# Optimization experiments

Hardware: AMD Instinct MI355X
Metric: run time of the kernel (lower is better)

## Reference

```python
import jax, jax.numpy as jnp
import numpy as np

B, N, D, H = 4, 4096, 512, 8
K = D // H  # per-head dim = 64


def setup_inputs() -> dict:
    key = jax.random.key(0)
    k1, k2, k3, k4 = jax.random.split(key, 4)
    x = jax.random.normal(k1, (B, N, D), dtype=jnp.float32)
    # Conv1d(D, K, 1, bias=False) -> weight matrix [K, D], kaiming fan_out
    Wa = jax.random.normal(k2, (K, D), dtype=jnp.float32) * np.float32(np.sqrt(2.0 / K))
    # Conv1d(K, 1, 1) -> weight vector [K], bias scalar (init 0.01)
    Wb = jax.random.normal(k3, (K,), dtype=jnp.float32) * np.float32(np.sqrt(2.0))
    Wc = jax.random.normal(k4, (K,), dtype=jnp.float32) * np.float32(np.sqrt(2.0))
    wb_bias = jnp.full((), 0.01, dtype=jnp.float32)
    wc_bias = jnp.full((), 0.01, dtype=jnp.float32)
    bias = jnp.full((K,), 0.01, dtype=jnp.float32)
    return {"batchinput": x, "Wa": Wa, "Wb": Wb, "wb_bias": wb_bias,
            "Wc": Wc, "wc_bias": wc_bias, "bias": bias}


def reference(batchinput, Wa, Wb, wb_bias, Wc, wc_bias, bias):
    # single step (n_steps=1); all n_head heads share weights, so mean over
    # identical heads equals one head (dropout=0.0 -> identity).
    h = jnp.einsum('bnd,kd->bnk', batchinput, Wa)            # [B,N,K] projected feats
    t1 = jnp.einsum('bnk,k->bn', h, Wb) + wb_bias            # [B,N]
    t2 = jnp.einsum('bnk,k->bn', h, Wc) + wc_bias            # [B,N]
    scores = t1[:, :, None] + t2[:, None, :]                 # [B,N,N] additive score
    coefs = jax.nn.softmax(jax.nn.leaky_relu(scores, negative_slope=0.2), axis=-1)
    out = jnp.einsum('bnm,bmk->bnk', coefs, h) + bias        # [B,N,K]
    return out
```

## Files before the change

### kernel.cpp

```cpp
#include <hip/hip_runtime.h>
#include <hip/hip_bf16.h>

constexpr int cB = 4;
constexpr int cN = 4096;
constexpr int cD = 512;
constexpr int cK = 64;
constexpr int cNB = cB * cN;
constexpr int cNP = cN + 1;
constexpr int cCS = 16;
constexpr int cNC = cN / cCS;
constexpr int cNC1 = cNC + 1;

typedef unsigned short u16;
typedef unsigned int u32;
typedef unsigned long long u64;
typedef __bf16 bf16x8 __attribute__((ext_vector_type(8)));
typedef float f32x4 __attribute__((ext_vector_type(4)));

constexpr size_t OFF_H    = 0;
constexpr size_t OFF_T1   = OFF_H    + (size_t)cNB * cK;
constexpr size_t OFF_T2   = OFF_T1   + cNB;
constexpr size_t OFF_T2S  = OFF_T2   + cNB;
constexpr size_t OFF_IDX  = OFF_T2S  + cNB;
constexpr size_t OFF_EPL  = OFF_IDX  + cNB;
constexpr size_t OFF_GNL  = OFF_EPL  + (size_t)cB * cNP * cK;
constexpr size_t OFF_EPS  = OFF_GNL  + (size_t)cB * cNP * cK;
constexpr size_t OFF_GNS  = OFF_EPS  + (size_t)cB * cNP;
constexpr size_t OFF_CHE  = OFF_GNS  + (size_t)cB * cNP;
constexpr size_t OFF_CHG  = OFF_CHE  + (size_t)cB * cNC * cK;
constexpr size_t OFF_CHES = OFF_CHG  + (size_t)cB * cNC * cK;
constexpr size_t OFF_CHGS = OFF_CHES + (size_t)cB * cNC;
constexpr size_t OFF_OFE  = OFF_CHGS + (size_t)cB * cNC;
constexpr size_t OFF_OFG  = OFF_OFE  + (size_t)cB * cNC1 * cK;
constexpr size_t OFF_OFES = OFF_OFG  + (size_t)cB * cNC1 * cK;
constexpr size_t OFF_OFGS = OFF_OFES + (size_t)cB * cNC1;
constexpr size_t OFF_XB16 = OFF_OFGS + (size_t)cB * cNC1;
constexpr size_t OFF_WB16 = OFF_XB16 + (size_t)cNB * cD / 2;

__device__ __forceinline__ u16 f2bf(float f) {
    unsigned u = __float_as_uint(f);
    u += 0x7fffu + ((u >> 16) & 1u);
    return (u16)(u >> 16);
}
__device__ __forceinline__ u32 pk2(float a, float b) {
    return (u32)f2bf(a) | ((u32)f2bf(b) << 16);
}
__device__ __forceinline__ u32 f2sort(float f) {
    u32 b = __float_as_uint(f);
    u32 mask = (u32)((int)b >> 31);
    return b ^ (mask | 0x80000000u);
}

__global__ __launch_bounds__(256) void k_prep(
    const float* __restrict__ x, const float* __restrict__ Wa,
    const float* __restrict__ Wb, const float* __restrict__ wbb,
    const float* __restrict__ Wc, const float* __restrict__ wcb,
    u16* __restrict__ xb16, u16* __restrict__ wab16,
    float* __restrict__ t1, float* __restrict__ t2)
{
    __shared__ float wabL[cD], wacL[cD];
    int t = threadIdx.x;
    if (blockIdx.x >= 512) {
        int i4 = (((int)blockIdx.x - 512) * 256 + t) * 4;
        float4 v = *(const float4*)(Wa + i4);
        uint2 p = {pk2(v.x, v.y), pk2(v.z, v.w)};
        *(uint2*)(wab16 + i4) = p;
        return;
    }
    float s1a = 0.f, s2a = 0.f, s1b = 0.f, s2b = 0.f;
#pragma unroll 8
    for (int k = 0; k < cK; ++k) {
        float wbk = Wb[k], wck = Wc[k];
        float wa1 = Wa[k * cD + t];
        float wa2 = Wa[k * cD + t + 256];
        s1a += wa1 * wbk; s2a += wa1 * wck;
        s1b += wa2 * wbk; s2b += wa2 * wck;
    }
    wabL[t] = s1a; wacL[t] = s2a; wabL[t + 256] = s1b; wacL[t + 256] = s2b;
    __syncthreads();

    int w = t >> 6, lane = t & 63;
    int d1 = lane * 4, d2 = 256 + lane * 4;
    float4 wbA = *(const float4*)&wabL[d1], wbB = *(const float4*)&wabL[d2];
    float4 wcA = *(const float4*)&wacL[d1], wcB = *(const float4*)&wacL[d2];
    float wbbv = wbb[0], wcbv = wcb[0];
#pragma unroll 2
    for (int rr = 0; rr < 8; ++rr) {
        int row = blockIdx.x * 32 + w * 8 + rr;
        const float* xp = x + (size_t)row * cD;
        float4 a  = *(const float4*)(xp + d1);
        float4 bq = *(const float4*)(xp + d2);
        uint2 pa = {pk2(a.x, a.y), pk2(a.z, a.w)};
        uint2 pb = {pk2(bq.x, bq.y), pk2(bq.z, bq.w)};
        *(uint2*)(xb16 + (size_t)row * cD + d1) = pa;
        *(uint2*)(xb16 + (size_t)row * cD + d2) = pb;
        float p1 = a.x*wbA.x + a.y*wbA.y + a.z*wbA.z + a.w*wbA.w
                 + bq.x*wbB.x + bq.y*wbB.y + bq.z*wbB.z + bq.w*wbB.w;
        float p2 = a.x*wcA.x + a.y*wcA.y + a.z*wcA.z + a.w*wcA.w
                 + bq.x*wcB.x + bq.y*wcB.y + bq.z*wcB.z + bq.w*wcB.w;
#pragma unroll
        for (int off = 32; off > 0; off >>= 1) {
            p1 += __shfl_down(p1, off, 64);
            p2 += __shfl_down(p2, off, 64);
        }
        if (lane == 0) { t1[row] = p1 + wbbv; t2[row] = p2 + wcbv; }
    }
}

__global__ __launch_bounds__(256) void k_projrank(
    const u16* __restrict__ xb16, const u16* __restrict__ wab16,
    const float* __restrict__ t2,
    float* __restrict__ h, float* __restrict__ t2s, int* __restrict__ idxs)
{
    __shared__ u64 shbuf[4096 + 128];
    int t = threadIdx.x;
    if (blockIdx.x < 256) {
        u16* xs = (u16*)shbuf;
        u16* was = xs + 64 * 32;
        int rowbase = blockIdx.x * 64;
        int w = t >> 6, lane = t & 63, m = lane & 15, quad = lane >> 4;
        int grow = w * 16 + (lane >> 2);
        int gcol = (lane & 3) * 8;
        const u16* xg = xb16 + (size_t)(rowbase + grow) * cD + gcol;
        const u16* wg = wab16 + (size_t)grow * cD + gcol;
        int lidx = grow * 32 + gcol;

        f32x4 acc[4] = {{0.f,0.f,0.f,0.f},{0.f,0.f,0.f,0.f},
                        {0.f,0.f,0.f,0.f},{0.f,0.f,0.f,0.f}};
        uint4 xv = *(const uint4*)(xg);
        uint4 wv = *(const uint4*)(wg);
        for (int s = 0; s < 16; ++s) {
            __syncthreads();
            *(uint4*)&xs[lidx] = xv;
            *(uint4*)&was[lidx] = wv;
            if (s < 15) {
                xv = *(const uint4*)(xg + (s + 1) * 32);
                wv = *(const uint4*)(wg + (s + 1) * 32);
            }
            __syncthreads();
            bf16x8 av = *(const bf16x8*)&xs[(w * 16 + m) * 32 + quad * 8];
#pragma unroll
            for (int g = 0; g < 4; ++g) {
                bf16x8 bv = *(const bf16x8*)&was[(g * 16 + m) * 32 + quad * 8];
                acc[g] = __builtin_amdgcn_mfma_f32_16x16x32_bf16(av, bv, acc[g], 0, 0, 0);
            }
        }
#pragma unroll
        for (int g = 0; g < 4; ++g) {
#pragma unroll
            for (int r4 = 0; r4 < 4; ++r4) {
                int row = w * 16 + quad * 4 + r4;
                h[(size_t)(rowbase + row) * cK + g * 16 + m] = acc[g][r4];
            }
        }
    } else {
        u64* keys = shbuf;
        int* part = (int*)(shbuf + 4096);
        int rb = blockIdx.x - 256;
        int b = rb >> 6;
        int rowgrp = rb & 63;
        for (int i = t; i < cN; i += 256)
            keys[i] = ((u64)f2sort(t2[b * cN + i]) << 32) | (u32)i;
        __syncthreads();
        int lane = t & 63, subset = t >> 6;
        u64 mykey = keys[rowgrp * 64 + lane];
        int s0 = subset * 1024;
        int cnt = 0;
#pragma unroll 8
        for (int kk = 0; kk < 1024; ++kk)
            cnt += (keys[s0 + kk] < mykey) ? 1 : 0;
        part[subset * 64 + lane] = cnt;
        __syncthreads();
        if (t < 64) {
            int jj = rowgrp * 64 + t;
            int rank = part[t] + part[64 + t] + part[128 + t] + part[192 + t];
            t2s[b * cN + rank] = t2[b * cN + jj];
            idxs[b * cN + rank] = jj;
        }
    }
}

__global__ __launch_bounds__(64) void k_chunkscan(
    const float* __restrict__ t2s, const int* __restrict__ idxs,
    const float* __restrict__ h,
    float* __restrict__ EpL, float* __restrict__ GnL,
    float* __restrict__ eps_l, float* __restrict__ gns_l,
    float* __restrict__ chE, float* __restrict__ chG,
    float* __restrict__ chEs, float* __restrict__ chGs)
{
    int lane = threadIdx.x;
    int blk = blockIdx.x;
    int c = blk & (cNC - 1);
    int b = blk >> 8;
    int base = b * cN + c * cCS;
    size_t rowbase = ((size_t)b * cNP + c * cCS) * cK;
    int sbase = b * cNP + c * cCS;
    float M2 = t2s[b * cN + cN - 1];
    int   idxv = (lane < cCS) ? idxs[base + lane] : 0;
    float t2v  = (lane < cCS) ? t2s[base + lane] : 0.f;

    float hv[cCS];
#pragma unroll
    for (int i = 0; i < cCS; ++i) {
        int j = __shfl(idxv, i, 64);
        hv[i] = h[((size_t)b * cN + j) * cK + lane];
    }
    float ee[cCS], gg[cCS];
#pragma unroll
    for (int i = 0; i < cCS; ++i) {
        float d = __shfl(t2v, i, 64) - M2;
        ee[i] = __expf(d);
        gg[i] = __expf(0.2f * d);
    }
    if (c == cNC - 1) {
        EpL[((size_t)b * cNP + cN) * cK + lane] = 0.f;
        GnL[((size_t)b * cNP + cN) * cK + lane] = 0.f;
        if (lane == 0) { eps_l[b * cNP + cN] = 0.f; gns_l[b * cNP + cN] = 0.f; }
    }
    float acc = 0.f, accs = 0.f;
#pragma unroll
    for (int i = cCS - 1; i >= 0; --i) {
        acc += ee[i] * hv[i]; accs += ee[i];
        EpL[rowbase + (size_t)i * cK + lane] = acc;
        if (lane == 0) eps_l[sbase + i] = accs;
    }
    chE[((size_t)b * cNC + c) * cK + lane] = acc;
    if (lane == 0) chEs[b * cNC + c] = accs;
    acc = 0.f; accs = 0.f;
#pragma unroll
    for (int i = 0; i < cCS; ++i) {
        GnL[rowbase + (size_t)i * cK + lane] = acc;
        if (lane == 0) gns_l[sbase + i] = accs;
        acc += gg[i] * hv[i]; accs += gg[i];
    }
    chG[((size_t)b * cNC + c) * cK + lane] = acc;
    if (lane == 0) chGs[b * cNC + c] = accs;
}

__global__ __launch_bounds__(256) void k_offsets(
    const float* __restrict__ chE, const float* __restrict__ chG,
    const float* __restrict__ chEs, const float* __restrict__ chGs,
    float* __restrict__ ofE, float* __restrict__ ofG,
    float* __restrict__ ofEs, float* __restrict__ ofGs)
{
    __shared__ float wsum[4][64];
    int t = threadIdx.x;
    int lane = t & 63, w = t >> 6;
    int dir = blockIdx.x & 1;
    int b = blockIdx.x >> 1;
    const float* ch = dir ? chG : chE;
    float* of = dir ? ofG : ofE;
    int c0 = w * 64;

    float cv[64];
    float s = 0.f;
#pragma unroll
    for (int i = 0; i < 64; ++i) {
        cv[i] = ch[((size_t)b * cNC + c0 + i) * cK + lane];
        s += cv[i];
    }
    wsum[w][lane] = s;
    __syncthreads();
    float base = 0.f;
    if (dir == 0) { for (int w2 = w + 1; w2 < 4; ++w2) base += wsum[w2][lane]; }
    else          { for (int w2 = 0; w2 < w; ++w2) base += wsum[w2][lane]; }

    if (dir == 0) {
        float run = base;
#pragma unroll
        for (int i = 63; i >= 0; --i) {
            of[((size_t)b * cNC1 + c0 + i) * cK + lane] = run;
            run += cv[i];
        }
        if (w == 0) of[((size_t)b * cNC1 + cNC) * cK + lane] = 0.f;
    } else {
        float run = base;
#pragma unroll
        for (int i = 0; i < 64; ++i) {
            of[((size_t)b * cNC1 + c0 + i) * cK + lane] = run;
            run += cv[i];
        }
        if (w == 3) of[((size_t)b * cNC1 + cNC) * cK + lane] = run;
    }

    if (w == 0) {
        const float* chs = dir ? chGs : chEs;
        float* ofs = dir ? ofGs : ofEs;
        float e0 = chs[b * cNC + lane * 4 + 0];
        float e1 = chs[b * cNC + lane * 4 + 1];
        float e2 = chs[b * cNC + lane * 4 + 2];
        float e3 = chs[b * cNC + lane * 4 + 3];
        float p = e0 + e1 + e2 + e3;
        if (dir == 0) {
            float s2 = p;
#pragma unroll
            for (int off = 1; off < 64; off <<= 1) {
                float tv = __shfl_down(s2, off, 64);
                if (lane + off < 64) s2 += tv;
            }
            float excl = s2 - p;
            ofs[b * cNC1 + lane * 4 + 0] = excl + e1 + e2 + e3;
            ofs[b * cNC1 + lane * 4 + 1] = excl + e2 + e3;
            ofs[b * cNC1 + lane * 4 + 2] = excl + e3;
            ofs[b * cNC1 + lane * 4 + 3] = excl;
            if (lane == 0) ofs[b * cNC1 + cNC] = 0.f;
        } else {
            float s2 = p;
#pragma unroll
            for (int off = 1; off < 64; off <<= 1) {
                float tv = __shfl_up(s2, off, 64);
                if (lane >= off) s2 += tv;
            }
            float excl = s2 - p;
            ofs[b * cNC1 + lane * 4 + 0] = excl;
            ofs[b * cNC1 + lane * 4 + 1] = excl + e0;
            ofs[b * cNC1 + lane * 4 + 2] = excl + e0 + e1;
            ofs[b * cNC1 + lane * 4 + 3] = excl + e0 + e1 + e2;
            if (lane == 63) ofs[b * cNC1 + cNC] = s2;
        }
    }
}

__global__ __launch_bounds__(256) void k_out(
    const float* __restrict__ t1, const float* __restrict__ t2s,
    const float* __restrict__ EpL, const float* __restrict__ GnL,
    const float* __restrict__ eps_l, const float* __restrict__ gns_l,
    const float* __restrict__ ofE, const float* __restrict__ ofG,
    const float* __restrict__ ofEs, const float* __restrict__ ofGs,
    const float* __restrict__ bias, float* __restrict__ out)
{
    int tid = threadIdx.x;
    int lane = tid & 63;
    int r = blockIdx.x * 4 + (tid >> 6);
    int b = r >> 12;
    float T1 = t1[r];
    float M2 = t2s[b * cN + cN - 1];
    float smax = T1 + M2;
    float m = fmaxf(smax, 0.2f * smax);
    float A  = __expf(smax - m);
    float Cc = __expf(0.2f * smax - m);
    float keyv = -T1;
    int lo = 0, hi = cN;
    while (lo < hi) {
        int mid = (lo + hi) >> 1;
        if (t2s[b * cN + mid] < keyv) lo = mid + 1; else hi = mid;
    }
    int p = lo;
    int c = p >> 4;
    size_t pr = ((size_t)b * cNP + p) * cK + lane;
    size_t cr = ((size_t)b * cNC1 + c) * cK + lane;
    float num = A * (EpL[pr] + ofE[cr]) + Cc * (GnL[pr] + ofG[cr]);
    float den = A * (eps_l[(size_t)b * cNP + p] + ofEs[b * cNC1 + c])
              + Cc * (gns_l[(size_t)b * cNP + p] + ofGs[b * cNC1 + c]);
    out[(size_t)r * cK + lane] = num / den + bias[lane];
}

extern "C" void kernel_launch(void* const* d_in, const int* in_sizes, int n_in,
                              void* d_out, int out_size, void* d_ws, size_t ws_size,
                              hipStream_t stream)
{
    const float* x    = (const float*)d_in[0];
    const float* Wa   = (const float*)d_in[1];
    const float* Wb   = (const float*)d_in[2];
    const float* wbb  = (const float*)d_in[3];
    const float* Wc   = (const float*)d_in[4];
    const float* wcb  = (const float*)d_in[5];
    const float* bias = (const float*)d_in[6];
    float* out = (float*)d_out;

    float* ws = (float*)d_ws;
    float* h     = ws + OFF_H;
    float* t1    = ws + OFF_T1;
    float* t2    = ws + OFF_T2;
    float* t2s   = ws + OFF_T2S;
    int*   idxs  = (int*)(ws + OFF_IDX);
    float* EpL   = ws + OFF_EPL;
    float* GnL   = ws + OFF_GNL;
    float* eps_l = ws + OFF_EPS;
    float* gns_l = ws + OFF_GNS;
    float* chE   = ws + OFF_CHE;
    float* chG   = ws + OFF_CHG;
    float* chEs  = ws + OFF_CHES;
    float* chGs  = ws + OFF_CHGS;
    float* ofE   = ws + OFF_OFE;
    float* ofG   = ws + OFF_OFG;
    float* ofEs  = ws + OFF_OFES;
    float* ofGs  = ws + OFF_OFGS;
    u16*   xb16  = (u16*)(ws + OFF_XB16);
    u16*   wab16 = (u16*)(ws + OFF_WB16);

    k_prep<<<544, 256, 0, stream>>>(x, Wa, Wb, wbb, Wc, wcb, xb16, wab16, t1, t2);
    k_projrank<<<512, 256, 0, stream>>>(xb16, wab16, t2, h, t2s, idxs);
    k_chunkscan<<<cB * cNC, 64, 0, stream>>>(t2s, idxs, h, EpL, GnL, eps_l, gns_l,
                                             chE, chG, chEs, chGs);
    k_offsets<<<cB * 2, 256, 0, stream>>>(chE, chG, chEs, chGs, ofE, ofG, ofEs, ofGs);
    k_out<<<cNB / 4, 256, 0, stream>>>(t1, t2s, EpL, GnL, eps_l, gns_l,
                                       ofE, ofG, ofEs, ofGs, bias, out);
}
```

Measured before the change: 132.3 us.

## Rank via wave ballots, precompute search positions, widen scan and offset kernels

The rank blocks stop staging keys in LDS and each thread holds 16 keys in registers. Ranks are counted with ballot and popcount against rows broadcast by readlane. The same pass also computes each row's insertion position for -t1, so k_out drops its per-row binary search over t2s. k_chunkscan now splits the forward and backward scans across two waves sharing h through LDS, and k_offsets uses 16 waves instead of 4. The cost is more ballot work in the rank kernel and one extra index array in the workspace.

```diff
diff --git a/kernel.cpp b/kernel.cpp
--- a/kernel.cpp
+++ b/kernel.cpp
@@ -22,7 +22,8 @@
 constexpr size_t OFF_T2   = OFF_T1   + cNB;
 constexpr size_t OFF_T2S  = OFF_T2   + cNB;
 constexpr size_t OFF_IDX  = OFF_T2S  + cNB;
-constexpr size_t OFF_EPL  = OFF_IDX  + cNB;
+constexpr size_t OFF_P    = OFF_IDX  + cNB;
+constexpr size_t OFF_EPL  = OFF_P    + cNB;
 constexpr size_t OFF_GNL  = OFF_EPL  + (size_t)cB * cNP * cK;
 constexpr size_t OFF_EPS  = OFF_GNL  + (size_t)cB * cNP * cK;
 constexpr size_t OFF_GNS  = OFF_EPS  + (size_t)cB * cNP;
@@ -109,10 +110,11 @@
 
 __global__ __launch_bounds__(256) void k_projrank(
     const u16* __restrict__ xb16, const u16* __restrict__ wab16,
-    const float* __restrict__ t2,
-    float* __restrict__ h, float* __restrict__ t2s, int* __restrict__ idxs)
-{
-    __shared__ u64 shbuf[4096 + 128];
+    const float* __restrict__ t1, const float* __restrict__ t2,
+    float* __restrict__ h, float* __restrict__ t2s, int* __restrict__ idxs,
+    int* __restrict__ pidx)
+{
+    __shared__ __align__(16) u64 shbuf[1024];
     int t = threadIdx.x;
     if (blockIdx.x < 256) {
         u16* xs = (u16*)shbuf;
@@ -154,33 +156,58 @@
             }
         }
     } else {
-        u64* keys = shbuf;
-        int* part = (int*)(shbuf + 4096);
+        int* part = (int*)shbuf;
         int rb = blockIdx.x - 256;
         int b = rb >> 6;
         int rowgrp = rb & 63;
-        for (int i = t; i < cN; i += 256)
-            keys[i] = ((u64)f2sort(t2[b * cN + i]) << 32) | (u32)i;
-        __syncthreads();
-        int lane = t & 63, subset = t >> 6;
-        u64 mykey = keys[rowgrp * 64 + lane];
-        int s0 = subset * 1024;
-        int cnt = 0;
+        int lane = t & 63, w = t >> 6;
+        int rowbase = rowgrp * 64;
+        const float* t2b = t2 + (size_t)b * cN;
+        u64 kk[16];
+        int jbase = t * 16;
+#pragma unroll
+        for (int i = 0; i < 16; i += 4) {
+            float4 v = *(const float4*)(t2b + jbase + i);
+            kk[i+0] = ((u64)f2sort(v.x) << 32) | (u32)(jbase + i + 0);
+            kk[i+1] = ((u64)f2sort(v.y) << 32) | (u32)(jbase + i + 1);
+            kk[i+2] = ((u64)f2sort(v.z) << 32) | (u32)(jbase + i + 2);
+            kk[i+3] = ((u64)f2sort(v.w) << 32) | (u32)(jbase + i + 3);
+        }
+        int myrow = rowbase + lane;
+        float t2r = t2b[myrow];
+        u64 rowkey = ((u64)f2sort(t2r) << 32) | (u32)myrow;
+        u32 rk_lo = (u32)rowkey, rk_hi = (u32)(rowkey >> 32);
+        u32 pk_hi = f2sort(-t1[(size_t)b * cN + myrow]);
+        int rankAcc = 0, pAcc = 0;
 #pragma unroll 8
-        for (int kk = 0; kk < 1024; ++kk)
-            cnt += (keys[s0 + kk] < mykey) ? 1 : 0;
-        part[subset * 64 + lane] = cnt;
+        for (int r = 0; r < 64; ++r) {
+            u32 tlo = (u32)__builtin_amdgcn_readlane((int)rk_lo, r);
+            u32 thi = (u32)__builtin_amdgcn_readlane((int)rk_hi, r);
+            u32 tph = (u32)__builtin_amdgcn_readlane((int)pk_hi, r);
+            u64 thr = ((u64)thi << 32) | tlo;
+            int c1 = 0, c2 = 0;
+#pragma unroll
+            for (int i = 0; i < 16; ++i) {
+                c1 += (int)__popcll(__ballot(kk[i] < thr));
+                c2 += (int)__popcll(__ballot((u32)(kk[i] >> 32) < tph));
+            }
+            if (lane == r) { rankAcc = c1; pAcc = c2; }
+        }
+        part[w * 64 + lane] = rankAcc;
+        part[256 + w * 64 + lane] = pAcc;
         __syncthreads();
         if (t < 64) {
-            int jj = rowgrp * 64 + t;
+            int row = rowbase + t;
             int rank = part[t] + part[64 + t] + part[128 + t] + part[192 + t];
-            t2s[b * cN + rank] = t2[b * cN + jj];
-            idxs[b * cN + rank] = jj;
-        }
-    }
-}
-
-__global__ __launch_bounds__(64) void k_chunkscan(
+            int pc   = part[256 + t] + part[320 + t] + part[384 + t] + part[448 + t];
+            t2s[(size_t)b * cN + rank] = t2b[row];
+            idxs[(size_t)b * cN + rank] = row;
+            pidx[(size_t)b * cN + row] = pc;
+        }
+    }
+}
+
+__global__ __launch_bounds__(128) void k_chunkscan(
     const float* __restrict__ t2s, const int* __restrict__ idxs,
     const float* __restrict__ h,
     float* __restrict__ EpL, float* __restrict__ GnL,
@@ -188,7 +215,9 @@
     float* __restrict__ chE, float* __restrict__ chG,
     float* __restrict__ chEs, float* __restrict__ chGs)
 {
-    int lane = threadIdx.x;
+    __shared__ float hs[cCS][cK];
+    int t = threadIdx.x;
+    int lane = t & 63, w = t >> 6;
     int blk = blockIdx.x;
     int c = blk & (cNC - 1);
     int b = blk >> 8;
@@ -196,79 +225,85 @@
     size_t rowbase = ((size_t)b * cNP + c * cCS) * cK;
     int sbase = b * cNP + c * cCS;
     float M2 = t2s[b * cN + cN - 1];
-    int   idxv = (lane < cCS) ? idxs[base + lane] : 0;
+    int   idxv = (lane < 8) ? idxs[base + w * 8 + lane] : 0;
     float t2v  = (lane < cCS) ? t2s[base + lane] : 0.f;
 
-    float hv[cCS];
-#pragma unroll
-    for (int i = 0; i < cCS; ++i) {
-        int j = __shfl(idxv, i, 64);
-        hv[i] = h[((size_t)b * cN + j) * cK + lane];
-    }
-    float ee[cCS], gg[cCS];
-#pragma unroll
-    for (int i = 0; i < cCS; ++i) {
-        float d = __shfl(t2v, i, 64) - M2;
-        ee[i] = __expf(d);
-        gg[i] = __expf(0.2f * d);
-    }
+#pragma unroll
+    for (int ii = 0; ii < 8; ++ii) {
+        int i = w * 8 + ii;
+        int j = __shfl(idxv, ii, 64);
+        hs[i][lane] = h[((size_t)b * cN + j) * cK + lane];
+    }
+    float slope = w ? 0.2f : 1.0f;
+    float ev[cCS];
+#pragma unroll
+    for (int i = 0; i < cCS; ++i)
+        ev[i] = __expf(slope * (__shfl(t2v, i, 64) - M2));
+    __syncthreads();
+
     if (c == cNC - 1) {
-        EpL[((size_t)b * cNP + cN) * cK + lane] = 0.f;
-        GnL[((size_t)b * cNP + cN) * cK + lane] = 0.f;
-        if (lane == 0) { eps_l[b * cNP + cN] = 0.f; gns_l[b * cNP + cN] = 0.f; }
+        if (w == 0) {
+            EpL[((size_t)b * cNP + cN) * cK + lane] = 0.f;
+            if (lane == 0) eps_l[b * cNP + cN] = 0.f;
+        } else {
+            GnL[((size_t)b * cNP + cN) * cK + lane] = 0.f;
+            if (lane == 0) gns_l[b * cNP + cN] = 0.f;
+        }
     }
     float acc = 0.f, accs = 0.f;
-#pragma unroll
-    for (int i = cCS - 1; i >= 0; --i) {
-        acc += ee[i] * hv[i]; accs += ee[i];
-        EpL[rowbase + (size_t)i * cK + lane] = acc;
-        if (lane == 0) eps_l[sbase + i] = accs;
-    }
-    chE[((size_t)b * cNC + c) * cK + lane] = acc;
-    if (lane == 0) chEs[b * cNC + c] = accs;
-    acc = 0.f; accs = 0.f;
-#pragma unroll
-    for (int i = 0; i < cCS; ++i) {
-        GnL[rowbase + (size_t)i * cK + lane] = acc;
-        if (lane == 0) gns_l[sbase + i] = accs;
-        acc += gg[i] * hv[i]; accs += gg[i];
-    }
-    chG[((size_t)b * cNC + c) * cK + lane] = acc;
-    if (lane == 0) chGs[b * cNC + c] = accs;
-}
-
-__global__ __launch_bounds__(256) void k_offsets(
+    if (w == 0) {
+#pragma unroll
+        for (int i = cCS - 1; i >= 0; --i) {
+            acc += ev[i] * hs[i][lane]; accs += ev[i];
+            EpL[rowbase + (size_t)i * cK + lane] = acc;
+            if (lane == 0) eps_l[sbase + i] = accs;
+        }
+        chE[((size_t)b * cNC + c) * cK + lane] = acc;
+        if (lane == 0) chEs[b * cNC + c] = accs;
+    } else {
+#pragma unroll
+        for (int i = 0; i < cCS; ++i) {
+            GnL[rowbase + (size_t)i * cK + lane] = acc;
+            if (lane == 0) gns_l[sbase + i] = accs;
+            acc += ev[i] * hs[i][lane]; accs += ev[i];
+        }
+        chG[((size_t)b * cNC + c) * cK + lane] = acc;
+        if (lane == 0) chGs[b * cNC + c] = accs;
+    }
+}
+
+__global__ __launch_bounds__(1024) void k_offsets(
     const float* __restrict__ chE, const float* __restrict__ chG,
     const float* __restrict__ chEs, const float* __restrict__ chGs,
     float* __restrict__ ofE, float* __restrict__ ofG,
     float* __restrict__ ofEs, float* __restrict__ ofGs)
 {
-    __shared__ float wsum[4][64];
+    __shared__ float wsum[16][64];
     int t = threadIdx.x;
     int lane = t & 63, w = t >> 6;
     int dir = blockIdx.x & 1;
     int b = blockIdx.x >> 1;
     const float* ch = dir ? chG : chE;
     float* of = dir ? ofG : ofE;
-    int c0 = w * 64;
-
-    float cv[64];
+    int c0 = w * 16;
+
+    float cv[16];
     float s = 0.f;
 #pragma unroll
-    for (int i = 0; i < 64; ++i) {
+    for (int i = 0; i < 16; ++i) {
         cv[i] = ch[((size_t)b * cNC + c0 + i) * cK + lane];
         s += cv[i];
     }
     wsum[w][lane] = s;
     __syncthreads();
     float base = 0.f;
-    if (dir == 0) { for (int w2 = w + 1; w2 < 4; ++w2) base += wsum[w2][lane]; }
+    if (dir == 0) { for (int w2 = w + 1; w2 < 16; ++w2) base += wsum[w2][lane]; }
     else          { for (int w2 = 0; w2 < w; ++w2) base += wsum[w2][lane]; }
 
     if (dir == 0) {
         float run = base;
 #pragma unroll
-        for (int i = 63; i >= 0; --i) {
+        for (int i = 15; i >= 0; --i) {
             of[((size_t)b * cNC1 + c0 + i) * cK + lane] = run;
             run += cv[i];
         }
@@ -276,11 +311,11 @@
     } else {
         float run = base;
 #pragma unroll
-        for (int i = 0; i < 64; ++i) {
+        for (int i = 0; i < 16; ++i) {
             of[((size_t)b * cNC1 + c0 + i) * cK + lane] = run;
             run += cv[i];
         }
-        if (w == 3) of[((size_t)b * cNC1 + cNC) * cK + lane] = run;
+        if (w == 15) of[((size_t)b * cNC1 + cNC) * cK + lane] = run;
     }
 
     if (w == 0) {
@@ -323,6 +358,7 @@
 
 __global__ __launch_bounds__(256) void k_out(
     const float* __restrict__ t1, const float* __restrict__ t2s,
+    const int* __restrict__ pidx,
     const float* __restrict__ EpL, const float* __restrict__ GnL,
     const float* __restrict__ eps_l, const float* __restrict__ gns_l,
     const float* __restrict__ ofE, const float* __restrict__ ofG,
@@ -339,13 +375,7 @@
     float m = fmaxf(smax, 0.2f * smax);
     float A  = __expf(smax - m);
     float Cc = __expf(0.2f * smax - m);
-    float keyv = -T1;
-    int lo = 0, hi = cN;
-    while (lo < hi) {
-        int mid = (lo + hi) >> 1;
-        if (t2s[b * cN + mid] < keyv) lo = mid + 1; else hi = mid;
-    }
-    int p = lo;
+    int p = pidx[r];
     int c = p >> 4;
     size_t pr = ((size_t)b * cNP + p) * cK + lane;
     size_t cr = ((size_t)b * cNC1 + c) * cK + lane;
@@ -374,6 +404,7 @@
     float* t2    = ws + OFF_T2;
     float* t2s   = ws + OFF_T2S;
     int*   idxs  = (int*)(ws + OFF_IDX);
+    int*   pidx  = (int*)(ws + OFF_P);
     float* EpL   = ws + OFF_EPL;
     float* GnL   = ws + OFF_GNL;
     float* eps_l = ws + OFF_EPS;
@@ -390,10 +421,10 @@
     u16*   wab16 = (u16*)(ws + OFF_WB16);
 
     k_prep<<<544, 256, 0, stream>>>(x, Wa, Wb, wbb, Wc, wcb, xb16, wab16, t1, t2);
-    k_projrank<<<512, 256, 0, stream>>>(xb16, wab16, t2, h, t2s, idxs);
-    k_chunkscan<<<cB * cNC, 64, 0, stream>>>(t2s, idxs, h, EpL, GnL, eps_l, gns_l,
-                                             chE, chG, chEs, chGs);
-    k_offsets<<<cB * 2, 256, 0, stream>>>(chE, chG, chEs, chGs, ofE, ofG, ofEs, ofGs);
-    k_out<<<cNB / 4, 256, 0, stream>>>(t1, t2s, EpL, GnL, eps_l, gns_l,
+    k_projrank<<<512, 256, 0, stream>>>(xb16, wab16, t1, t2, h, t2s, idxs, pidx);
+    k_chunkscan<<<cB * cNC, 128, 0, stream>>>(t2s, idxs, h, EpL, GnL, eps_l, gns_l,
+                                              chE, chG, chEs, chGs);
+    k_offsets<<<cB * 2, 1024, 0, stream>>>(chE, chG, chEs, chGs, ofE, ofG, ofEs, ofGs);
+    k_out<<<cNB / 4, 256, 0, stream>>>(t1, t2s, pidx, EpL, GnL, eps_l, gns_l,
                                        ofE, ofG, ofEs, ofGs, bias, out);
 }
```

Result: slower. 144.0 us (+8.8%).
